# Kernel optimization log

Measured on AMD Instinct MI355X. Metric: run time of the kernel, lower is better.

Reference implementation:

```python
import jax, jax.numpy as jnp
import numpy as np

N = 100000        # nodes
E = 1_600_000     # edges (avg degree 16)
F_IN = 128        # in_channels
HID = 64          # hidden_channels (per-head)
H1 = 4            # heads layer 1
G = 128           # number of graphs
NEG_SLOPE = 0.2   # PyG GATConv default leaky_relu slope


def setup_inputs() -> dict:
    key = jax.random.key(0)
    ks = jax.random.split(key, 12)
    x = jax.random.normal(ks[0], (N, F_IN), dtype=jnp.float32)
    edge_index = jax.random.randint(ks[1], (2, E), 0, N, dtype=jnp.int64)
    batch = jnp.sort(jax.random.randint(ks[2], (N,), 0, G, dtype=jnp.int64))
    s1 = 1.0 / np.sqrt(F_IN)
    s2 = 1.0 / np.sqrt(H1 * HID)
    # layer 1: in=F_IN, out=H1*HID (PyG lin has no bias; separate bias after concat)
    w1 = jax.random.normal(ks[3], (H1 * HID, F_IN), dtype=jnp.float32) * s1
    a_src1 = jax.random.normal(ks[4], (H1, HID), dtype=jnp.float32) * s1
    a_dst1 = jax.random.normal(ks[5], (H1, HID), dtype=jnp.float32) * s1
    b1 = jnp.zeros((H1 * HID,), dtype=jnp.float32)
    # layer 2: in=H1*HID, out=HID, heads=1
    w2 = jax.random.normal(ks[6], (1 * HID, H1 * HID), dtype=jnp.float32) * s2
    a_src2 = jax.random.normal(ks[7], (1, HID), dtype=jnp.float32) * s2
    a_dst2 = jax.random.normal(ks[8], (1, HID), dtype=jnp.float32) * s2
    b2 = jnp.zeros((HID,), dtype=jnp.float32)
    return {"x": x, "w1": w1, "a_src1": a_src1, "a_dst1": a_dst1, "b1": b1,
            "w2": w2, "a_src2": a_src2, "a_dst2": a_dst2, "b2": b2,
            "edge_index": edge_index, "batch": batch}


def _segment_softmax(alpha, seg, n):
    # numerically-stable softmax of alpha [E,H] grouped by seg (dst node)
    m = jax.ops.segment_max(alpha, seg, num_segments=n)
    m = jnp.where(jnp.isfinite(m), m, 0.0)  # empty segments -> 0
    a = jnp.exp(alpha - m[seg])
    s = jax.ops.segment_sum(a, seg, num_segments=n)
    return a / (s[seg] + 1e-16)


def _gat_conv(x, w, a_src, a_dst, bias, src, dst, n, heads, ch):
    h = (x @ w.T).reshape(n, heads, ch)          # [N,H,C]
    alpha_src = jnp.sum(h * a_src[None], axis=-1)  # [N,H]
    alpha_dst = jnp.sum(h * a_dst[None], axis=-1)  # [N,H]
    e = jax.nn.leaky_relu(alpha_src[src] + alpha_dst[dst], NEG_SLOPE)  # [E,H]
    att = _segment_softmax(e, dst, n)             # [E,H]
    msg = h[src] * att[:, :, None]                # [E,H,C]
    out = jax.ops.segment_sum(msg, dst, num_segments=n)  # [N,H,C]
    return out.reshape(n, heads * ch) + bias


def reference(x, w1, a_src1, a_dst1, b1, w2, a_src2, a_dst2, b2, edge_index, batch):
    src, dst = edge_index[0], edge_index[1]
    h = jax.nn.relu(_gat_conv(x, w1, a_src1, a_dst1, b1, src, dst, N, H1, HID))
    h = jax.nn.relu(_gat_conv(h, w2, a_src2, a_dst2, b2, src, dst, N, 1, HID))
    # global_mean_pool over graph ids
    sums = jax.ops.segment_sum(h, batch, num_segments=G)            # [G,HID]
    cnt = jax.ops.segment_sum(jnp.ones((N,), h.dtype), batch, num_segments=G)
    return sums / jnp.maximum(cnt, 1.0)[:, None]
```

## Files before the change

### kernel.cpp

```cpp
#include <hip/hip_runtime.h>
#include <math.h>
#include <type_traits>

#define NNODES 100000
#define NEDGES 1600000
#define NGRAPH 128
#define NBKT 391
#define CAP 1536
#define EPB 2048

typedef _Float16 f16x4 __attribute__((ext_vector_type(4)));
typedef _Float16 f16x8 __attribute__((ext_vector_type(8)));
typedef float f32x4 __attribute__((ext_vector_type(4)));

template <int K, int N, typename AT>
__global__ __launch_bounds__(256, 2) void gemm_mfma(const AT* __restrict__ A,
    const float* __restrict__ B, _Float16* __restrict__ C, int M,
    const float* __restrict__ a_src, const float* __restrict__ a_dst,
    float* __restrict__ asrc, float* __restrict__ adst) {
  constexpr int BM = 64;
  constexpr int H = N / 64;
  __shared__ _Float16 As[BM * K];
  __shared__ _Float16 Bs[N * K];
  const int tid = threadIdx.x;
  const int bm = blockIdx.x * BM;

  for (int i = tid * 4; i < BM * K; i += 1024) {
    int row = i / K;
    int k = i & (K - 1);
    int gr = bm + row;
    f16x4 h;
    if constexpr (std::is_same<AT, float>::value) {
      float4 v = {0.f, 0.f, 0.f, 0.f};
      if (gr < M) v = *(const float4*)&A[(size_t)gr * K + k];
      h[0] = (_Float16)v.x; h[1] = (_Float16)v.y; h[2] = (_Float16)v.z; h[3] = (_Float16)v.w;
    } else {
      f16x4 v = {};
      if (gr < M) v = *(const f16x4*)&A[(size_t)gr * K + k];
      h = v;
    }
    int idx = (row * K + k) ^ ((row & 7) << 3);
    *(f16x4*)&As[idx] = h;
  }
  for (int i = tid * 4; i < N * K; i += 1024) {
    int row = i / K;
    int k = i & (K - 1);
    float4 v = *(const float4*)&B[(size_t)row * K + k];
    f16x4 h;
    h[0] = (_Float16)v.x; h[1] = (_Float16)v.y; h[2] = (_Float16)v.z; h[3] = (_Float16)v.w;
    int idx = (row * K + k) ^ ((row & 7) << 3);
    *(f16x4*)&Bs[idx] = h;
  }
  __syncthreads();

  const int lane = tid & 63, wid = tid >> 6;
  const int lr = lane & 15;
  const int lk = (lane >> 4) * 8;
  constexpr int KS = K / 32, NT = N / 16;

  f16x8 a[KS];
#pragma unroll
  for (int ks = 0; ks < KS; ++ks) {
    int row = wid * 16 + lr;
    int idx = (row * K + ks * 32 + lk) ^ ((row & 7) << 3);
    a[ks] = *(const f16x8*)&As[idx];
  }

  f32x4 acc[NT];
#pragma unroll
  for (int nt = 0; nt < NT; ++nt) acc[nt] = (f32x4){0.f, 0.f, 0.f, 0.f};

#pragma unroll
  for (int nt = 0; nt < NT; ++nt)
#pragma unroll
    for (int ks = 0; ks < KS; ++ks) {
      int row = nt * 16 + lr;
      int idx = (row * K + ks * 32 + lk) ^ ((row & 7) << 3);
      f16x8 b = *(const f16x8*)&Bs[idx];
      acc[nt] = __builtin_amdgcn_mfma_f32_16x16x32_f16(a[ks], b, acc[nt], 0, 0, 0);
    }

  float cs[NT], cd[NT];
#pragma unroll
  for (int nt = 0; nt < NT; ++nt) {
    cs[nt] = a_src[nt * 16 + lr];
    cd[nt] = a_dst[nt * 16 + lr];
  }

  int row0 = bm + wid * 16 + (lane >> 4) * 4;
#pragma unroll
  for (int r = 0; r < 4; ++r) {
    int row = row0 + r;
    float ps[H], pd[H];
#pragma unroll
    for (int h = 0; h < H; ++h) { ps[h] = 0.f; pd[h] = 0.f; }
#pragma unroll
    for (int nt = 0; nt < NT; ++nt) {
      int h = nt >> 2;
      if (H == 1) h = 0;
      ps[h] = fmaf(acc[nt][r], cs[nt], ps[h]);
      pd[h] = fmaf(acc[nt][r], cd[nt], pd[h]);
    }
#pragma unroll
    for (int o = 1; o < 16; o <<= 1) {
#pragma unroll
      for (int h = 0; h < H; ++h) {
        ps[h] += __shfl_xor(ps[h], o);
        pd[h] += __shfl_xor(pd[h], o);
      }
    }
    if (row < M) {
#pragma unroll
      for (int nt = 0; nt < NT; ++nt) C[(size_t)row * N + nt * 16 + lr] = (_Float16)acc[nt][r];
      if (lr == 0) {
        if (H == 4) {
          *(float4*)&asrc[row * 4] = make_float4(ps[0], ps[1], ps[2], ps[3 % H]);
          *(float4*)&adst[row * 4] = make_float4(pd[0], pd[1], pd[2], pd[3 % H]);
        } else {
          asrc[row] = ps[0];
          adst[row] = pd[0];
        }
      }
    }
  }
}

__global__ __launch_bounds__(256) void bucketA(const int* __restrict__ srcv,
    const int* __restrict__ dstv, int2* __restrict__ part, int* __restrict__ gcur,
    int e_count) {
  __shared__ int hist[NBKT];
  __shared__ int base_[NBKT];
  __shared__ int lofs[NBKT];
  const int tid = threadIdx.x;
  const int P = blockIdx.x & 7;
  for (int i = tid; i < NBKT; i += 256) { hist[i] = 0; lofs[i] = 0; }
  __syncthreads();
  const int e0 = blockIdx.x * EPB;
  const int e1 = min(e0 + EPB, e_count);
  for (int e = e0 + tid; e < e1; e += 256) atomicAdd(&hist[dstv[e] >> 8], 1);
  __syncthreads();
  for (int i = tid; i < NBKT; i += 256) {
    int c = hist[i];
    base_[i] = c ? atomicAdd(&gcur[(P * NBKT + i) * 16], c) : 0;
  }
  __syncthreads();
  for (int e = e0 + tid; e < e1; e += 256) {
    int d = dstv[e];
    int b = d >> 8;
    int l = atomicAdd(&lofs[b], 1);
    part[(size_t)(P * NBKT + b) * CAP + base_[b] + l] = make_int2(srcv[e], d);
  }
}

__global__ __launch_bounds__(256) void bucketB1(const int2* __restrict__ part,
    const int* __restrict__ gcur, int* __restrict__ deg, int n) {
  __shared__ int cnt[256];
  const int b = blockIdx.x;
  const int tid = threadIdx.x;
  cnt[tid] = 0;
  __syncthreads();
  for (int P = 0; P < 8; ++P) {
    int cn = gcur[(P * NBKT + b) * 16];
    const int2* seg = part + (size_t)(P * NBKT + b) * CAP;
    for (int i = tid; i < cn; i += 256) atomicAdd(&cnt[seg[i].y & 255], 1);
  }
  __syncthreads();
  int node = (b << 8) + tid;
  if (node < n) deg[node] = cnt[tid];
}

__global__ __launch_bounds__(256) void bucketB2(const int2* __restrict__ part,
    const int* __restrict__ gcur, const int* __restrict__ offsets,
    int* __restrict__ esrc, int n) {
  __shared__ int lcur[256];
  const int b = blockIdx.x;
  const int tid = threadIdx.x;
  int node = (b << 8) + tid;
  lcur[tid] = (node < n) ? offsets[node] : 0;
  __syncthreads();
  for (int P = 0; P < 8; ++P) {
    int cn = gcur[(P * NBKT + b) * 16];
    const int2* seg = part + (size_t)(P * NBKT + b) * CAP;
    for (int i = tid; i < cn; i += 256) {
      int2 e = seg[i];
      int slot = atomicAdd(&lcur[e.y & 255], 1);
      esrc[slot] = e.x;
    }
  }
}

__global__ __launch_bounds__(1024) void scan1(const int* __restrict__ deg, int* __restrict__ inc,
                                              int* __restrict__ bsum, int n) {
  __shared__ int sm[1024];
  int i = blockIdx.x * 1024 + threadIdx.x;
  sm[threadIdx.x] = (i < n) ? deg[i] : 0;
  __syncthreads();
  for (int o = 1; o < 1024; o <<= 1) {
    int t = (threadIdx.x >= o) ? sm[threadIdx.x - o] : 0;
    __syncthreads();
    sm[threadIdx.x] += t;
    __syncthreads();
  }
  if (i < n) inc[i] = sm[threadIdx.x];
  if (threadIdx.x == 1023) bsum[blockIdx.x] = sm[1023];
}

__global__ void scan2(const int* __restrict__ bsum, int* __restrict__ boff, int nb) {
  __shared__ int sm[128];
  int t = threadIdx.x;
  int own = (t < nb) ? bsum[t] : 0;
  sm[t] = own;
  __syncthreads();
  for (int o = 1; o < 128; o <<= 1) {
    int u = (t >= o) ? sm[t - o] : 0;
    __syncthreads();
    sm[t] += u;
    __syncthreads();
  }
  if (t < nb) boff[t] = sm[t] - own;
}

__global__ void scan3(const int* __restrict__ inc, const int* __restrict__ deg,
                      const int* __restrict__ boff, int* __restrict__ offsets,
                      int n, int e_count) {
  int i = blockIdx.x * blockDim.x + threadIdx.x;
  if (i < n) offsets[i] = inc[i] - deg[i] + boff[i >> 10];
  if (i == 0) offsets[n] = e_count;
}

__global__ __launch_bounds__(256) void agg1_kernel(const _Float16* __restrict__ hmat,
    const float* __restrict__ asrc, const float* __restrict__ adst,
    const int* __restrict__ offsets, const int* __restrict__ esrc,
    const float* __restrict__ bias, _Float16* __restrict__ outv, int node0, int node_end) {
  const int lane = threadIdx.x & 63, wid = threadIdx.x >> 6;
  const int node = node0 + blockIdx.x * 4 + wid;
  if (node >= node_end) return;
  const int h = lane >> 4;
  const int start = offsets[node];
  const int end = offsets[node + 1];
  const float adn = adst[node * 4 + h];
  const _Float16* hbase = hmat + lane * 4;
  float acc[4] = {0.f, 0.f, 0.f, 0.f};
  float s = 0.f;
  int j = start;
  for (; j + 8 <= end; j += 8) {
    int sv[8];
#pragma unroll
    for (int t = 0; t < 8; ++t) sv[t] = esrc[j + t];
    f16x4 vv[8];
#pragma unroll
    for (int t = 0; t < 8; ++t) vv[t] = *(const f16x4*)&hbase[(size_t)sv[t] * 256];
    _Float16 ph[8];
#pragma unroll
    for (int t = 0; t < 8; ++t) {
      float v = asrc[sv[t] * 4 + h] + adn;
      v = (v > 0.f) ? v : 0.2f * v;
      float p = __expf(v);
      s += p;
      ph[t] = (_Float16)p;
    }
#pragma unroll
    for (int t = 0; t < 8; ++t)
#pragma unroll
      for (int k = 0; k < 4; ++k)
        acc[k] = fmaf((float)vv[t][k], (float)ph[t], acc[k]);
  }
  for (; j < end; ++j) {
    int sv = esrc[j];
    f16x4 vv = *(const f16x4*)&hbase[(size_t)sv * 256];
    float v = asrc[sv * 4 + h] + adn;
    v = (v > 0.f) ? v : 0.2f * v;
    float p = __expf(v);
    s += p;
    _Float16 phs = (_Float16)p;
#pragma unroll
    for (int k = 0; k < 4; ++k) acc[k] = fmaf((float)vv[k], (float)phs, acc[k]);
  }
  float inv = 1.f / (s + 1e-16f);
  f16x4 ho;
#pragma unroll
  for (int k = 0; k < 4; ++k)
    ho[k] = (_Float16)fmaxf(fmaf(acc[k], inv, bias[lane * 4 + k]), 0.f);
  *(f16x4*)&outv[(size_t)node * 256 + lane * 4] = ho;
}

__global__ __launch_bounds__(256) void agg2_kernel(const _Float16* __restrict__ hmat,
    const float* __restrict__ asrc, const float* __restrict__ adst,
    const int* __restrict__ offsets, const int* __restrict__ esrc,
    const float* __restrict__ bias, float* __restrict__ outv) {
  const int lane = threadIdx.x & 63, wid = threadIdx.x >> 6;
  const int g = lane >> 4, q = lane & 15;
  const int node = blockIdx.x * 16 + wid * 4 + g;
  if (node >= NNODES) return;
  const int start = offsets[node];
  const int end = offsets[node + 1];
  const float adn = adst[node];
  const _Float16* hbase = hmat + q * 4;
  float acc[4] = {0.f, 0.f, 0.f, 0.f};
  float s = 0.f;
  int j = start;
  for (; j + 4 <= end; j += 4) {
    int sv[4];
#pragma unroll
    for (int t = 0; t < 4; ++t) sv[t] = esrc[j + t];
    f16x4 v[4];
#pragma unroll
    for (int t = 0; t < 4; ++t) v[t] = *(const f16x4*)&hbase[(size_t)sv[t] * 64];
#pragma unroll
    for (int t = 0; t < 4; ++t) {
      float x = asrc[sv[t]] + adn;
      x = (x > 0.f) ? x : 0.2f * x;
      float p = __expf(x);
      s += p;
      _Float16 phs = (_Float16)p;
#pragma unroll
      for (int k = 0; k < 4; ++k) acc[k] = fmaf((float)v[t][k], (float)phs, acc[k]);
    }
  }
  for (; j < end; ++j) {
    int sv = esrc[j];
    f16x4 v = *(const f16x4*)&hbase[(size_t)sv * 64];
    float x = asrc[sv] + adn;
    x = (x > 0.f) ? x : 0.2f * x;
    float p = __expf(x);
    s += p;
    _Float16 phs = (_Float16)p;
#pragma unroll
    for (int k = 0; k < 4; ++k) acc[k] = fmaf((float)v[k], (float)phs, acc[k]);
  }
  float inv = 1.f / (s + 1e-16f);
  float4 o;
  o.x = fmaxf(fmaf(acc[0], inv, bias[q * 4 + 0]), 0.f);
  o.y = fmaxf(fmaf(acc[1], inv, bias[q * 4 + 1]), 0.f);
  o.z = fmaxf(fmaf(acc[2], inv, bias[q * 4 + 2]), 0.f);
  o.w = fmaxf(fmaf(acc[3], inv, bias[q * 4 + 3]), 0.f);
  *(float4*)&outv[(size_t)node * 64 + q * 4] = o;
}

__global__ __launch_bounds__(256) void pool_kernel(const float* __restrict__ g2,
    const int* __restrict__ batch, float* __restrict__ out, int n) {
  const int gid = blockIdx.x;
  const int lane = threadIdx.x & 63, w = threadIdx.x >> 6;
  int lo = 0, hi = n;
  while (lo < hi) { int mid = (lo + hi) >> 1; if (batch[mid] < gid) lo = mid + 1; else hi = mid; }
  int lb = lo;
  hi = n;
  while (lo < hi) { int mid = (lo + hi) >> 1; if (batch[mid] < gid + 1) lo = mid + 1; else hi = mid; }
  int ub = lo;
  float acc = 0.f;
  for (int i = lb + w; i < ub; i += 4) acc += g2[(size_t)i * 64 + lane];
  __shared__ float red[4][64];
  red[w][lane] = acc;
  __syncthreads();
  if (threadIdx.x < 64) {
    float sum = (red[0][lane] + red[1][lane]) + (red[2][lane] + red[3][lane]);
    float cnt = fmaxf((float)(ub - lb), 1.f);
    out[gid * 64 + lane] = sum / cnt;
  }
}

extern "C" void kernel_launch(void* const* d_in, const int* in_sizes, int n_in,
                              void* d_out, int out_size, void* d_ws, size_t ws_size,
                              hipStream_t stream) {
  const float* x      = (const float*)d_in[0];
  const float* w1     = (const float*)d_in[1];
  const float* a_src1 = (const float*)d_in[2];
  const float* a_dst1 = (const float*)d_in[3];
  const float* b1     = (const float*)d_in[4];
  const float* w2     = (const float*)d_in[5];
  const float* a_src2 = (const float*)d_in[6];
  const float* a_dst2 = (const float*)d_in[7];
  const float* b2     = (const float*)d_in[8];
  const int*   src    = (const int*)d_in[9];
  const int*   dst    = src + NEDGES;
  const int*   batch  = (const int*)d_in[10];
  float* out = (float*)d_out;

  const int N = NNODES, E = NEDGES;
  const int NB = (N + 1023) / 1024;

  char* wsb = (char*)d_ws;
  size_t off = 0;
  auto alloc = [&](size_t bytes) {
    void* p = wsb + off;
    off = (off + bytes + 255) & ~(size_t)255;
    return p;
  };
  _Float16* h1h = (_Float16*)alloc((size_t)N * 256 * 2);
  _Float16* g1h = (_Float16*)alloc((size_t)N * 256 * 2);
  _Float16* h2h = (_Float16*)alloc((size_t)N * 64 * 2);
  float* g2     = (float*)alloc((size_t)N * 64 * 4);
  float* as1    = (float*)alloc((size_t)N * 4 * 4);
  float* ad1    = (float*)alloc((size_t)N * 4 * 4);
  float* as2    = (float*)alloc((size_t)N * 4);
  float* ad2    = (float*)alloc((size_t)N * 4);
  int* deg      = (int*)alloc((size_t)N * 4);
  int* inc      = (int*)alloc((size_t)N * 4);
  int* bsum     = (int*)alloc((size_t)NB * 4);
  int* boff     = (int*)alloc((size_t)NB * 4);
  int* offsets  = (int*)alloc((size_t)(N + 1) * 4);
  int* esrc     = (int*)alloc((size_t)E * 4);
  int2* part    = (int2*)alloc((size_t)8 * NBKT * CAP * 8);
  int* gcur     = (int*)alloc((size_t)8 * NBKT * 16 * 4);

  hipMemsetAsync(gcur, 0, (size_t)8 * NBKT * 16 * 4, stream);
  bucketA<<<(E + EPB - 1) / EPB, 256, 0, stream>>>(src, dst, part, gcur, E);
  bucketB1<<<NBKT, 256, 0, stream>>>(part, gcur, deg, N);
  scan1<<<NB, 1024, 0, stream>>>(deg, inc, bsum, N);
  scan2<<<1, 128, 0, stream>>>(bsum, boff, NB);
  scan3<<<(N + 255) / 256, 256, 0, stream>>>(inc, deg, boff, offsets, N, E);
  bucketB2<<<NBKT, 256, 0, stream>>>(part, gcur, offsets, esrc, N);

  gemm_mfma<128, 256, float><<<(N + 63) / 64, 256, 0, stream>>>(
      x, w1, h1h, N, a_src1, a_dst1, as1, ad1);
  agg1_kernel<<<8334, 256, 0, stream>>>(h1h, as1, ad1, offsets, esrc, b1, g1h, 0, 33336);
  agg1_kernel<<<8334, 256, 0, stream>>>(h1h, as1, ad1, offsets, esrc, b1, g1h, 33336, 66672);
  agg1_kernel<<<8332, 256, 0, stream>>>(h1h, as1, ad1, offsets, esrc, b1, g1h, 66672, 100000);

  gemm_mfma<256, 64, _Float16><<<(N + 63) / 64, 256, 0, stream>>>(
      g1h, w2, h2h, N, a_src2, a_dst2, as2, ad2);
  agg2_kernel<<<(N + 15) / 16, 256, 0, stream>>>(h2h, as2, ad2, offsets, esrc, b2, g2);

  pool_kernel<<<NGRAPH, 256, 0, stream>>>(g2, batch, out, N);
}
```

Before: 410.4 us.

## Pre-convert weights to fp16 and drop LDS staging in GEMMs, split N across blocks

Adds a small kernel that converts both weight matrices to fp16 once, so each GEMM block no longer converts the full fp32 weight matrix into shared memory. The GEMM now reads A fragments and B fragments directly from global memory into registers without LDS or a block barrier, and layer 1 splits the 256 output columns across two grid columns of 128. This removes per-block weight staging and conversion and reduces registers per thread. In exchange, B is reloaded from global/L2 per wave, A is read twice in layer 1, and the global loads are less coalesced.

```diff
diff --git a/kernel.cpp b/kernel.cpp
--- a/kernel.cpp
+++ b/kernel.cpp
@@ -13,57 +13,48 @@
 typedef _Float16 f16x8 __attribute__((ext_vector_type(8)));
 typedef float f32x4 __attribute__((ext_vector_type(4)));
 
-template <int K, int N, typename AT>
-__global__ __launch_bounds__(256, 2) void gemm_mfma(const AT* __restrict__ A,
-    const float* __restrict__ B, _Float16* __restrict__ C, int M,
+__global__ void convert_w(const float* __restrict__ w1, const float* __restrict__ w2,
+                          _Float16* __restrict__ w1h, _Float16* __restrict__ w2h) {
+  int i = blockIdx.x * 256 + threadIdx.x;
+  if (i < 256 * 128) w1h[i] = (_Float16)w1[i];
+  int j = i - 256 * 128;
+  if (j >= 0 && j < 64 * 256) w2h[j] = (_Float16)w2[j];
+}
+
+template <int K, int N, int BN, typename AT>
+__global__ __launch_bounds__(256) void gemm_mfma(const AT* __restrict__ A,
+    const _Float16* __restrict__ Bh, _Float16* __restrict__ C, int M,
     const float* __restrict__ a_src, const float* __restrict__ a_dst,
     float* __restrict__ asrc, float* __restrict__ adst) {
-  constexpr int BM = 64;
   constexpr int H = N / 64;
-  __shared__ _Float16 As[BM * K];
-  __shared__ _Float16 Bs[N * K];
-  const int tid = threadIdx.x;
-  const int bm = blockIdx.x * BM;
-
-  for (int i = tid * 4; i < BM * K; i += 1024) {
-    int row = i / K;
-    int k = i & (K - 1);
-    int gr = bm + row;
-    f16x4 h;
-    if constexpr (std::is_same<AT, float>::value) {
-      float4 v = {0.f, 0.f, 0.f, 0.f};
-      if (gr < M) v = *(const float4*)&A[(size_t)gr * K + k];
-      h[0] = (_Float16)v.x; h[1] = (_Float16)v.y; h[2] = (_Float16)v.z; h[3] = (_Float16)v.w;
-    } else {
-      f16x4 v = {};
-      if (gr < M) v = *(const f16x4*)&A[(size_t)gr * K + k];
-      h = v;
-    }
-    int idx = (row * K + k) ^ ((row & 7) << 3);
-    *(f16x4*)&As[idx] = h;
-  }
-  for (int i = tid * 4; i < N * K; i += 1024) {
-    int row = i / K;
-    int k = i & (K - 1);
-    float4 v = *(const float4*)&B[(size_t)row * K + k];
-    f16x4 h;
-    h[0] = (_Float16)v.x; h[1] = (_Float16)v.y; h[2] = (_Float16)v.z; h[3] = (_Float16)v.w;
-    int idx = (row * K + k) ^ ((row & 7) << 3);
-    *(f16x4*)&Bs[idx] = h;
-  }
-  __syncthreads();
-
-  const int lane = tid & 63, wid = tid >> 6;
+  constexpr int HB = BN / 64;
+  constexpr int KS = K / 32, NT = BN / 16;
+  const int lane = threadIdx.x & 63, wid = threadIdx.x >> 6;
   const int lr = lane & 15;
   const int lk = (lane >> 4) * 8;
-  constexpr int KS = K / 32, NT = N / 16;
+  const int row = blockIdx.x * 64 + wid * 16 + lr;
+  const int bn0 = blockIdx.y * BN;
+  const int hoff = blockIdx.y * HB;
 
   f16x8 a[KS];
-#pragma unroll
-  for (int ks = 0; ks < KS; ++ks) {
-    int row = wid * 16 + lr;
-    int idx = (row * K + ks * 32 + lk) ^ ((row & 7) << 3);
-    a[ks] = *(const f16x8*)&As[idx];
+  if (row < M) {
+    const AT* arow = A + (size_t)row * K;
+#pragma unroll
+    for (int ks = 0; ks < KS; ++ks) {
+      if constexpr (std::is_same<AT, float>::value) {
+        float4 v0 = *(const float4*)&arow[ks * 32 + lk];
+        float4 v1 = *(const float4*)&arow[ks * 32 + lk + 4];
+        f16x8 t;
+        t[0] = (_Float16)v0.x; t[1] = (_Float16)v0.y; t[2] = (_Float16)v0.z; t[3] = (_Float16)v0.w;
+        t[4] = (_Float16)v1.x; t[5] = (_Float16)v1.y; t[6] = (_Float16)v1.z; t[7] = (_Float16)v1.w;
+        a[ks] = t;
+      } else {
+        a[ks] = *(const f16x8*)&arow[ks * 32 + lk];
+      }
+    }
+  } else {
+#pragma unroll
+    for (int ks = 0; ks < KS; ++ks) a[ks] = (f16x8){};
   }
 
   f32x4 acc[NT];
@@ -71,54 +62,52 @@
   for (int nt = 0; nt < NT; ++nt) acc[nt] = (f32x4){0.f, 0.f, 0.f, 0.f};
 
 #pragma unroll
-  for (int nt = 0; nt < NT; ++nt)
+  for (int nt = 0; nt < NT; ++nt) {
+    const _Float16* brow = Bh + (size_t)(bn0 + nt * 16 + lr) * K;
 #pragma unroll
     for (int ks = 0; ks < KS; ++ks) {
-      int row = nt * 16 + lr;
-      int idx = (row * K + ks * 32 + lk) ^ ((row & 7) << 3);
-      f16x8 b = *(const f16x8*)&Bs[idx];
+      f16x8 b = *(const f16x8*)&brow[ks * 32 + lk];
       acc[nt] = __builtin_amdgcn_mfma_f32_16x16x32_f16(a[ks], b, acc[nt], 0, 0, 0);
     }
+  }
 
   float cs[NT], cd[NT];
 #pragma unroll
   for (int nt = 0; nt < NT; ++nt) {
-    cs[nt] = a_src[nt * 16 + lr];
-    cd[nt] = a_dst[nt * 16 + lr];
-  }
-
-  int row0 = bm + wid * 16 + (lane >> 4) * 4;
+    cs[nt] = a_src[bn0 + nt * 16 + lr];
+    cd[nt] = a_dst[bn0 + nt * 16 + lr];
+  }
+
+  int row0 = blockIdx.x * 64 + wid * 16 + (lane >> 4) * 4;
 #pragma unroll
   for (int r = 0; r < 4; ++r) {
-    int row = row0 + r;
-    float ps[H], pd[H];
-#pragma unroll
-    for (int h = 0; h < H; ++h) { ps[h] = 0.f; pd[h] = 0.f; }
+    int orow = row0 + r;
+    float ps[HB], pd[HB];
+#pragma unroll
+    for (int h = 0; h < HB; ++h) { ps[h] = 0.f; pd[h] = 0.f; }
 #pragma unroll
     for (int nt = 0; nt < NT; ++nt) {
-      int h = nt >> 2;
-      if (H == 1) h = 0;
+      int h = (HB == 1) ? 0 : (nt >> 2);
       ps[h] = fmaf(acc[nt][r], cs[nt], ps[h]);
       pd[h] = fmaf(acc[nt][r], cd[nt], pd[h]);
     }
 #pragma unroll
     for (int o = 1; o < 16; o <<= 1) {
 #pragma unroll
-      for (int h = 0; h < H; ++h) {
+      for (int h = 0; h < HB; ++h) {
         ps[h] += __shfl_xor(ps[h], o);
         pd[h] += __shfl_xor(pd[h], o);
       }
     }
-    if (row < M) {
-#pragma unroll
-      for (int nt = 0; nt < NT; ++nt) C[(size_t)row * N + nt * 16 + lr] = (_Float16)acc[nt][r];
+    if (orow < M) {
+#pragma unroll
+      for (int nt = 0; nt < NT; ++nt)
+        C[(size_t)orow * N + bn0 + nt * 16 + lr] = (_Float16)acc[nt][r];
       if (lr == 0) {
-        if (H == 4) {
-          *(float4*)&asrc[row * 4] = make_float4(ps[0], ps[1], ps[2], ps[3 % H]);
-          *(float4*)&adst[row * 4] = make_float4(pd[0], pd[1], pd[2], pd[3 % H]);
-        } else {
-          asrc[row] = ps[0];
-          adst[row] = pd[0];
+#pragma unroll
+        for (int h = 0; h < HB; ++h) {
+          asrc[orow * H + hoff + h] = ps[h];
+          adst[orow * H + hoff + h] = pd[h];
         }
       }
     }
@@ -402,6 +391,10 @@
   int* esrc     = (int*)alloc((size_t)E * 4);
   int2* part    = (int2*)alloc((size_t)8 * NBKT * CAP * 8);
   int* gcur     = (int*)alloc((size_t)8 * NBKT * 16 * 4);
+  _Float16* w1h = (_Float16*)alloc((size_t)256 * 128 * 2);
+  _Float16* w2h = (_Float16*)alloc((size_t)64 * 256 * 2);
+
+  convert_w<<<192, 256, 0, stream>>>(w1, w2, w1h, w2h);
 
   hipMemsetAsync(gcur, 0, (size_t)8 * NBKT * 16 * 4, stream);
   bucketA<<<(E + EPB - 1) / EPB, 256, 0, stream>>>(src, dst, part, gcur, E);
@@ -411,14 +404,20 @@
   scan3<<<(N + 255) / 256, 256, 0, stream>>>(inc, deg, boff, offsets, N, E);
   bucketB2<<<NBKT, 256, 0, stream>>>(part, gcur, offsets, esrc, N);
 
-  gemm_mfma<128, 256, float><<<(N + 63) / 64, 256, 0, stream>>>(
-      x, w1, h1h, N, a_src1, a_dst1, as1, ad1);
+  {
+    dim3 g((N + 63) / 64, 2);
+    gemm_mfma<128, 256, 128, float><<<g, 256, 0, stream>>>(
+        x, w1h, h1h, N, a_src1, a_dst1, as1, ad1);
+  }
   agg1_kernel<<<8334, 256, 0, stream>>>(h1h, as1, ad1, offsets, esrc, b1, g1h, 0, 33336);
   agg1_kernel<<<8334, 256, 0, stream>>>(h1h, as1, ad1, offsets, esrc, b1, g1h, 33336, 66672);
   agg1_kernel<<<8332, 256, 0, stream>>>(h1h, as1, ad1, offsets, esrc, b1, g1h, 66672, 100000);
 
-  gemm_mfma<256, 64, _Float16><<<(N + 63) / 64, 256, 0, stream>>>(
-      g1h, w2, h2h, N, a_src2, a_dst2, as2, ad2);
+  {
+    dim3 g((N + 63) / 64, 1);
+    gemm_mfma<256, 64, 64, _Float16><<<g, 256, 0, stream>>>(
+        g1h, w2h, h2h, N, a_src2, a_dst2, as2, ad2);
+  }
   agg2_kernel<<<(N + 15) / 16, 256, 0, stream>>>(h2h, as2, ad2, offsets, esrc, b2, g2);
 
   pool_kernel<<<NGRAPH, 256, 0, stream>>>(g2, batch, out, N);
```

Measured after the change: 414.2 us. No clear change (+0.9%).
